# Kernel optimization log

Hardware: AMD Instinct MI355X
Metric: run time of the kernel (lower is better)

The kernel has to match this reference:

```python
import math
import jax, jax.numpy as jnp
import numpy as np

LMAX = 2


def _cg_complex(j1, m1, j2, m2, j3, m3):
    # Standard (Racah) Clebsch-Gordan coefficient <j1 m1 j2 m2 | j3 m3> for integer l.
    if m1 + m2 != m3 or j3 < abs(j1 - j2) or j3 > j1 + j2:
        return 0.0
    f = math.factorial
    pre = math.sqrt((2 * j3 + 1) * f(j3 + j1 - j2) * f(j3 - j1 + j2) * f(j1 + j2 - j3) / f(j1 + j2 + j3 + 1))
    pre *= math.sqrt(f(j3 + m3) * f(j3 - m3) * f(j1 - m1) * f(j1 + m1) * f(j2 - m2) * f(j2 + m2))
    kmin = max(0, j2 - j3 - m1, j1 + m2 - j3)
    kmax = min(j1 + j2 - j3, j1 - m1, j2 + m2)
    s = 0.0
    for k in range(kmin, kmax + 1):
        s += (-1.0) ** k / (f(k) * f(j1 + j2 - j3 - k) * f(j1 - m1 - k) * f(j2 + m2 - k) * f(j3 - j2 + m1 + k) * f(j3 - j1 - m2 + k))
    return pre * s


def _u_matrix(l):
    # Unitary map from complex SH (Condon-Shortley) to real SH, rows = real mu, cols = complex m.
    U = np.zeros((2 * l + 1, 2 * l + 1), dtype=np.complex128)
    U[l, l] = 1.0
    isq2 = 1.0 / math.sqrt(2.0)
    for m in range(1, l + 1):
        U[l + m, l - m] = isq2
        U[l + m, l + m] = ((-1.0) ** m) * isq2
        U[l - m, l - m] = 1j * isq2
        U[l - m, l + m] = -1j * ((-1.0) ** m) * isq2
    return U


def _real_clebsch_gordan(lmax):
    # Dense real-SH CG tensor over combined s=(l,m) indices, shape [S,S,S], S=(lmax+1)^2.
    S = (lmax + 1) ** 2
    cg = np.zeros((S, S, S))
    for l1 in range(lmax + 1):
        for l2 in range(lmax + 1):
            for l3 in range(abs(l1 - l2), min(lmax, l1 + l2) + 1):
                blk = np.zeros((2 * l1 + 1, 2 * l2 + 1, 2 * l3 + 1))
                for i1, m1 in enumerate(range(-l1, l1 + 1)):
                    for i2, m2 in enumerate(range(-l2, l2 + 1)):
                        for i3, m3 in enumerate(range(-l3, l3 + 1)):
                            blk[i1, i2, i3] = _cg_complex(l1, m1, l2, m2, l3, m3)
                U1, U2, U3 = _u_matrix(l1), _u_matrix(l2), _u_matrix(l3)
                r = np.einsum('am,bn,co,mno->abc', U1, U2, U3.conj(), blk.astype(np.complex128))
                r = r.real if (l1 + l2 + l3) % 2 == 0 else r.imag  # parity-dependent real part
                cg[l1 * l1:(l1 + 1) ** 2, l2 * l2:(l2 + 1) ** 2, l3 * l3:(l3 + 1) ** 2] = r
    return cg


def _sparse_cg(lmax):
    cg = _real_clebsch_gordan(lmax)
    i1, i2, i3 = np.nonzero(np.abs(cg) > 1e-10)
    vals = cg[i1, i2, i3].astype(np.float32)
    widx = np.floor(np.sqrt(i3.astype(np.float64))).astype(np.int32)  # l of output combined index
    return vals, i1.astype(np.int32), i2.astype(np.int32), i3.astype(np.int32), widx


def _spherical_harmonics_l2(d):
    # Real SH up to l=2, 'component' normalization (|x|=1 assumed). Order: (l,m) = (0,0),(1,-1),(1,0),(1,1),(2,-2..2).
    x, y, z = d[..., 0], d[..., 1], d[..., 2]
    s3, s5, s15 = math.sqrt(3.0), math.sqrt(5.0), math.sqrt(15.0)
    return jnp.stack([
        jnp.ones_like(x),
        s3 * y, s3 * z, s3 * x,
        s15 * x * y, s15 * y * z, 0.5 * s5 * (3.0 * z * z - 1.0), s15 * x * z, 0.5 * s15 * (x * x - y * y),
    ], axis=-1)


def setup_inputs():
    N_ATOMS, N_EDGES, N_BASIS, N_RADIAL = 1200, 12000, 128, 20
    S = (LMAX + 1) ** 2
    key = jax.random.key(0)
    ks = jax.random.split(key, 8)
    vals, i1, i2, i3, widx = _sparse_cg(LMAX)
    return {
        'x': jax.random.normal(ks[0], (N_ATOMS, S, N_BASIS), jnp.float32),
        'radial_ij': jax.random.uniform(ks[1], (N_EDGES, N_RADIAL), jnp.float32),
        'dir_ij': jax.random.normal(ks[2], (N_EDGES, 3), jnp.float32),
        'cutoff_ij': jax.random.uniform(ks[3], (N_EDGES, 1), jnp.float32),
        'W_filter': jax.random.normal(ks[6], (N_RADIAL, N_BASIS * (LMAX + 1)), jnp.float32) / math.sqrt(N_RADIAL),
        'b_filter': jnp.zeros((N_BASIS * (LMAX + 1),), jnp.float32),
        'cg_vals': jnp.asarray(vals),
        'idx_i': jax.random.randint(ks[4], (N_EDGES,), 0, N_ATOMS),
        'idx_j': jax.random.randint(ks[5], (N_EDGES,), 0, N_ATOMS),
        'cg_idx_in1': jnp.asarray(i1),
        'cg_idx_in2': jnp.asarray(i2),
        'cg_idx_out': jnp.asarray(i3),
        'w_idx': jnp.asarray(widx),
    }


def reference(x, radial_ij, dir_ij, cutoff_ij, W_filter, b_filter, cg_vals,
              idx_i, idx_j, cg_idx_in1, cg_idx_in2, cg_idx_out, w_idx):
    n_atoms, S, F = x.shape
    E = dir_ij.shape[0]
    d = dir_ij / jnp.linalg.norm(dir_ij, axis=-1, keepdims=True)
    Y = _spherical_harmonics_l2(d)                        # [E, S]
    Wij = (radial_ij @ W_filter + b_filter) * cutoff_ij   # [E, (lmax+1)*F]
    Wij = Wij.reshape(E, LMAX + 1, F)                     # per-l radial filter
    xj = x[idx_j]                                         # [E, S, F] neighbor features
    # Sparse CG tensor-product contraction over combined (l,m) indices.
    v = (Y[:, cg_idx_in2, None] * cg_vals[None, :, None]
         * Wij[:, w_idx, :] * xj[:, cg_idx_in1, :])       # [E, n_cg, F]
    yij = jnp.zeros((E, S, F), v.dtype).at[:, cg_idx_out, :].add(v)
    return jax.ops.segment_sum(yij, idx_i, num_segments=n_atoms)
```

## Files before the change

### kernel.cpp

```cpp
#include <hip/hip_runtime.h>
#include <math.h>


#define S9     9
#define MROW   12
#define MSZ    (S9 * MROW)
#define NF     128
#define NRAD   20
#define CEDGE  8
#define NCHUNK 3
#define CAP    64
#define NCELL  81
#define MAXCG  512

__device__ inline float2 f2fma(float a, float2 b, float2 c) {
    return make_float2(fmaf(a, b.x, c.x), fmaf(a, b.y, c.y));
}

__global__ __launch_bounds__(256) void prep_kernel(
    const int* __restrict__ idx_i, int E, int nbuck,
    const int* __restrict__ cg_i1, const int* __restrict__ cg_i2,
    const int* __restrict__ cg_i3, const float* __restrict__ cg_vals, int ncg,
    int* __restrict__ cnt,
    int* __restrict__ buck,
    int* __restrict__ cellOff,
    int2* __restrict__ cellDat)
{
    const int t = threadIdx.x;
    if ((int)blockIdx.x < nbuck) {
        int e = blockIdx.x * 256 + t;
        if (e < E) {
            int a = idx_i[e];
            int p = atomicAdd(&cnt[a], 1);
            if (p < CAP) buck[a * CAP + p] = e;
        }
        return;
    }
    __shared__ int hist[NCELL];
    __shared__ int cur[NCELL];
    if (t < NCELL) hist[t] = 0;
    __syncthreads();
    for (int k = t; k < ncg; k += 256)
        atomicAdd(&hist[cg_i3[k] * S9 + cg_i1[k]], 1);
    __syncthreads();
    if (t == 0) {
        int run = 0;
        for (int c = 0; c < NCELL; ++c) {
            cellOff[c] = run; cur[c] = run; run += hist[c];
        }
        cellOff[NCELL] = run;
    }
    __syncthreads();
    for (int k = t; k < ncg; k += 256) {
        int cell = cg_i3[k] * S9 + cg_i1[k];
        int p = atomicAdd(&cur[cell], 1);
        cellDat[p] = make_int2(cg_i2[k], __float_as_int(cg_vals[k]));
    }
}

__global__ __launch_bounds__(64) void so3_chunk_kernel(
    const float* __restrict__ x,
    const float* __restrict__ radial,
    const float* __restrict__ dir,
    const float* __restrict__ cutoff,
    const float* __restrict__ Wf,
    const float* __restrict__ bf,
    const int* __restrict__ idx_j,
    const int* __restrict__ cnt,
    const int* __restrict__ buck,
    const int* __restrict__ cellOff,
    const int2* __restrict__ cellDat,
    int ncg,
    float* __restrict__ slots)
{
    const int a = blockIdx.x / NCHUNK;
    const int q = blockIdx.x - a * NCHUNK;
    const int t = threadIdx.x;

    const int deg = min(cnt[a], CAP);
    if (q > 0 && q * CEDGE >= deg) return;

    __shared__ __align__(16) float M[CEDGE][MSZ];
    __shared__ float Ysh[CEDGE][S9];
    __shared__ float radsh[CEDGE][NRAD];
    __shared__ float cutsh[CEDGE];
    __shared__ int   egsh[CEDGE];
    __shared__ int   jsh[CEDGE];
    __shared__ int   offsh[NCELL + 1];
    __shared__ int2  datsh[MAXCG];

    for (int k = t; k <= NCELL; k += 64) offsh[k] = cellOff[k];
    for (int k = t; k < ncg; k += 64) datsh[k] = cellDat[k];

    float2 acc[S9];
    #pragma unroll
    for (int s = 0; s < S9; ++s) acc[s] = make_float2(0.f, 0.f);

    const float2 b0 = ((const float2*)(bf + 0 * NF))[t];
    const float2 b1 = ((const float2*)(bf + 1 * NF))[t];
    const float2 b2 = ((const float2*)(bf + 2 * NF))[t];

    int base = q * CEDGE;
    do {
        const int n = min(CEDGE, deg - base);

        if (t < CEDGE) {
            int e = 0, jj = a;
            float cut = 0.f;
            float y0 = 0.f, y1 = 0.f, y2 = 0.f, y3 = 0.f, y4 = 0.f,
                  y5 = 0.f, y6 = 0.f, y7 = 0.f, y8 = 0.f;
            if (t < n) {
                e = buck[a * CAP + base + t];
                jj = idx_j[e];
                cut = cutoff[e];
                float dx = dir[3 * e], dy = dir[3 * e + 1], dz = dir[3 * e + 2];
                const float inv = rsqrtf(dx * dx + dy * dy + dz * dz);
                dx *= inv; dy *= inv; dz *= inv;
                const float s3c  = 1.7320508075688772f;
                const float s5c  = 2.2360679774997896f;
                const float s15c = 3.8729833462074170f;
                y0 = 1.0f;
                y1 = s3c * dy; y2 = s3c * dz; y3 = s3c * dx;
                y4 = s15c * dx * dy; y5 = s15c * dy * dz;
                y6 = 0.5f * s5c * (3.0f * dz * dz - 1.0f);
                y7 = s15c * dx * dz;
                y8 = 0.5f * s15c * (dx * dx - dy * dy);
            }
            egsh[t] = e; jsh[t] = jj; cutsh[t] = cut;
            Ysh[t][0] = y0; Ysh[t][1] = y1; Ysh[t][2] = y2;
            Ysh[t][3] = y3; Ysh[t][4] = y4; Ysh[t][5] = y5;
            Ysh[t][6] = y6; Ysh[t][7] = y7; Ysh[t][8] = y8;
        }
        for (int qq = t; qq < CEDGE * NRAD; qq += 64) {
            const int c = qq / NRAD;
            const int r = qq - c * NRAD;
            float v = 0.f;
            if (c < n) v = radial[(size_t)egsh[c] * NRAD + r];
            radsh[c][r] = v;
        }

        float2 w[CEDGE][3];
        #pragma unroll
        for (int c = 0; c < CEDGE; ++c) { w[c][0] = b0; w[c][1] = b1; w[c][2] = b2; }
        #pragma unroll 4
        for (int r = 0; r < NRAD; ++r) {
            const float2* wrow = (const float2*)(Wf + r * (3 * NF));
            const float2 w0 = wrow[t];
            const float2 w1 = wrow[t + 64];
            const float2 w2 = wrow[t + 128];
            #pragma unroll
            for (int c = 0; c < CEDGE; ++c) {
                const float rv = radsh[c][r];
                w[c][0] = f2fma(rv, w0, w[c][0]);
                w[c][1] = f2fma(rv, w1, w[c][1]);
                w[c][2] = f2fma(rv, w2, w[c][2]);
            }
        }
        #pragma unroll
        for (int c = 0; c < CEDGE; ++c) {
            const float cut = cutsh[c];
            w[c][0].x *= cut; w[c][0].y *= cut;
            w[c][1].x *= cut; w[c][1].y *= cut;
            w[c][2].x *= cut; w[c][2].y *= cut;
        }

        #pragma unroll
        for (int cc = 0; cc < 2; ++cc) {
            const int cell = t + cc * 64;
            if (cell < NCELL) {
                const int s3i = cell / 9;
                const int s1i = cell - 9 * s3i;
                const int o0 = offsh[cell], o1 = offsh[cell + 1];
                float m[CEDGE];
                #pragma unroll
                for (int c = 0; c < CEDGE; ++c) m[c] = 0.f;
                for (int idx = o0; idx < o1; ++idx) {
                    const int2 d = datsh[idx];
                    const float v = __int_as_float(d.y);
                    #pragma unroll
                    for (int c = 0; c < CEDGE; ++c)
                        m[c] = fmaf(v, Ysh[c][d.x], m[c]);
                }
                #pragma unroll
                for (int c = 0; c < CEDGE; ++c) M[c][s3i * MROW + s1i] = m[c];
            }
        }

        #pragma unroll
        for (int c = 0; c < CEDGE; ++c) {
            const int j = __builtin_amdgcn_readfirstlane(jsh[c]);
            const float2* xp = (const float2*)(x + (size_t)j * (S9 * NF)) + t;
            float2 xj[S9];
            #pragma unroll
            for (int s = 0; s < S9; ++s) xj[s] = xp[s * 64];

            #pragma unroll
            for (int s3 = 0; s3 < S9; ++s3) {
                const float4* mr = (const float4*)&M[c][s3 * MROW];
                const float4 m0 = mr[0];
                const float4 m1 = mr[1];
                const float  m8 = M[c][s3 * MROW + 8];
                float2 tsum = make_float2(0.f, 0.f);
                tsum = f2fma(m0.x, xj[0], tsum);
                tsum = f2fma(m0.y, xj[1], tsum);
                tsum = f2fma(m0.z, xj[2], tsum);
                tsum = f2fma(m0.w, xj[3], tsum);
                tsum = f2fma(m1.x, xj[4], tsum);
                tsum = f2fma(m1.y, xj[5], tsum);
                tsum = f2fma(m1.z, xj[6], tsum);
                tsum = f2fma(m1.w, xj[7], tsum);
                tsum = f2fma(m8,   xj[8], tsum);
                const float2 wl = (s3 == 0) ? w[c][0] : ((s3 < 4) ? w[c][1] : w[c][2]);
                acc[s3].x = fmaf(wl.x, tsum.x, acc[s3].x);
                acc[s3].y = fmaf(wl.y, tsum.y, acc[s3].y);
            }
        }
        base += CEDGE;
    } while (q == NCHUNK - 1 && base < deg);

    float2* sp = (float2*)(slots + (size_t)(a * NCHUNK + q) * (S9 * NF)) + t;
    #pragma unroll
    for (int s = 0; s < S9; ++s) sp[s * 64] = acc[s];
}

__global__ __launch_bounds__(64) void reduce_kernel(
    const float* __restrict__ slots, const int* __restrict__ cnt,
    float* __restrict__ out)
{
    const int a = blockIdx.x;
    const int t = threadIdx.x;
    const int deg = min(cnt[a], CAP);
    const int nch = min((deg + CEDGE - 1) / CEDGE, NCHUNK);

    float2 acc[S9];
    #pragma unroll
    for (int s = 0; s < S9; ++s) acc[s] = make_float2(0.f, 0.f);

    for (int q = 0; q < nch; ++q) {
        const float2* sp = (const float2*)(slots + (size_t)(a * NCHUNK + q) * (S9 * NF)) + t;
        #pragma unroll
        for (int s = 0; s < S9; ++s) {
            float2 v = sp[s * 64];
            acc[s].x += v.x; acc[s].y += v.y;
        }
    }
    float2* op = (float2*)(out + (size_t)a * (S9 * NF)) + t;
    #pragma unroll
    for (int s = 0; s < S9; ++s) op[s * 64] = acc[s];
}

__global__ __launch_bounds__(256) void so3_edge_fused(
    const float* __restrict__ x, const float* __restrict__ radial,
    const float* __restrict__ dir, const float* __restrict__ cutoff,
    const float* __restrict__ Wf, const float* __restrict__ bf,
    const float* __restrict__ cg_vals,
    const int* __restrict__ idx_i, const int* __restrict__ idx_j,
    const int* __restrict__ cg_i1, const int* __restrict__ cg_i2,
    const int* __restrict__ cg_i3, int ncg, int E,
    float* __restrict__ out)
{
    const int wid  = threadIdx.x >> 6;
    const int lane = threadIdx.x & 63;
    const int e = blockIdx.x * 4 + wid;
    if (e >= E) return;

    __shared__ __align__(16) float Msh[4][MSZ];
    __shared__ float Ysh[4][S9];

    if (lane < 27) ((float4*)&Msh[wid][0])[lane] = make_float4(0.f, 0.f, 0.f, 0.f);

    float dx = dir[3 * e], dy = dir[3 * e + 1], dz = dir[3 * e + 2];
    const float inv = rsqrtf(dx * dx + dy * dy + dz * dz);
    dx *= inv; dy *= inv; dz *= inv;
    if (lane == 0) {
        const float s3c = 1.7320508075688772f, s5c = 2.2360679774997896f,
                    s15c = 3.8729833462074170f;
        Ysh[wid][0] = 1.0f;
        Ysh[wid][1] = s3c * dy; Ysh[wid][2] = s3c * dz; Ysh[wid][3] = s3c * dx;
        Ysh[wid][4] = s15c * dx * dy; Ysh[wid][5] = s15c * dy * dz;
        Ysh[wid][6] = 0.5f * s5c * (3.0f * dz * dz - 1.0f);
        Ysh[wid][7] = s15c * dx * dz;
        Ysh[wid][8] = 0.5f * s15c * (dx * dx - dy * dy);
    }
    for (int k = lane; k < ncg; k += 64)
        atomicAdd(&Msh[wid][cg_i3[k] * MROW + cg_i1[k]], cg_vals[k] * Ysh[wid][cg_i2[k]]);

    float rad[NRAD];
    #pragma unroll
    for (int r = 0; r < NRAD; ++r) rad[r] = radial[(size_t)e * NRAD + r];
    const float cut = cutoff[e];

    float2 w0 = ((const float2*)(bf + 0 * NF))[lane];
    float2 w1 = ((const float2*)(bf + 1 * NF))[lane];
    float2 w2 = ((const float2*)(bf + 2 * NF))[lane];
    #pragma unroll 4
    for (int r = 0; r < NRAD; ++r) {
        const float2* wrow = (const float2*)(Wf + r * (3 * NF));
        w0 = f2fma(rad[r], wrow[lane], w0);
        w1 = f2fma(rad[r], wrow[lane + 64], w1);
        w2 = f2fma(rad[r], wrow[lane + 128], w2);
    }
    w0.x *= cut; w0.y *= cut; w1.x *= cut; w1.y *= cut; w2.x *= cut; w2.y *= cut;

    const int j = __builtin_amdgcn_readfirstlane(idx_j[e]);
    const float2* xp = (const float2*)(x + (size_t)j * (S9 * NF)) + lane;
    float2 xj[S9];
    #pragma unroll
    for (int s = 0; s < S9; ++s) xj[s] = xp[s * 64];

    const int a = __builtin_amdgcn_readfirstlane(idx_i[e]);
    float* op = out + (size_t)a * (S9 * NF) + 2 * lane;
    #pragma unroll
    for (int s3 = 0; s3 < S9; ++s3) {
        const float4* mr = (const float4*)&Msh[wid][s3 * MROW];
        const float4 m0 = mr[0];
        const float4 m1 = mr[1];
        const float  m8 = Msh[wid][s3 * MROW + 8];
        float2 tsum = make_float2(0.f, 0.f);
        tsum = f2fma(m0.x, xj[0], tsum);
        tsum = f2fma(m0.y, xj[1], tsum);
        tsum = f2fma(m0.z, xj[2], tsum);
        tsum = f2fma(m0.w, xj[3], tsum);
        tsum = f2fma(m1.x, xj[4], tsum);
        tsum = f2fma(m1.y, xj[5], tsum);
        tsum = f2fma(m1.z, xj[6], tsum);
        tsum = f2fma(m1.w, xj[7], tsum);
        tsum = f2fma(m8,   xj[8], tsum);
        const float2 wl = (s3 == 0) ? w0 : ((s3 < 4) ? w1 : w2);
        atomicAdd(&op[s3 * NF],     wl.x * tsum.x);
        atomicAdd(&op[s3 * NF + 1], wl.y * tsum.y);
    }
}

extern "C" void kernel_launch(void* const* d_in, const int* in_sizes, int n_in,
                              void* d_out, int out_size, void* d_ws, size_t ws_size,
                              hipStream_t stream) {
    const float* x       = (const float*)d_in[0];
    const float* radial  = (const float*)d_in[1];
    const float* dir     = (const float*)d_in[2];
    const float* cutoff  = (const float*)d_in[3];
    const float* Wf      = (const float*)d_in[4];
    const float* bf      = (const float*)d_in[5];
    const float* cg_vals = (const float*)d_in[6];
    const int*   idx_i   = (const int*)d_in[7];
    const int*   idx_j   = (const int*)d_in[8];
    const int*   cg_i1   = (const int*)d_in[9];
    const int*   cg_i2   = (const int*)d_in[10];
    const int*   cg_i3   = (const int*)d_in[11];

    const int E   = in_sizes[7];
    const int ncg = in_sizes[6];
    const int A   = in_sizes[0] / (S9 * NF);

    int* cnt      = (int*)d_ws;
    int* cellOff  = cnt + A;
    int* buck     = cellOff + (NCELL + 1);
    size_t ib     = (size_t)(A + NCELL + 1 + A * CAP) * sizeof(int);
    size_t doff   = (ib + 255) & ~(size_t)255;
    int2* cellDat = (int2*)((char*)d_ws + doff);
    size_t soff   = (doff + (size_t)ncg * sizeof(int2) + 255) & ~(size_t)255;
    float* slots  = (float*)((char*)d_ws + soff);
    size_t need   = soff + (size_t)A * NCHUNK * (S9 * NF) * sizeof(float);

    if (ws_size >= need && ncg <= MAXCG) {
        hipMemsetAsync(cnt, 0, (size_t)A * sizeof(int), stream);

        const int nbuck = (E + 255) / 256;
        prep_kernel<<<nbuck + 1, 256, 0, stream>>>(
            idx_i, E, nbuck, cg_i1, cg_i2, cg_i3, cg_vals, ncg,
            cnt, buck, cellOff, cellDat);

        so3_chunk_kernel<<<A * NCHUNK, 64, 0, stream>>>(
            x, radial, dir, cutoff, Wf, bf, idx_j,
            cnt, buck, cellOff, cellDat, ncg, slots);

        reduce_kernel<<<A, 64, 0, stream>>>(slots, cnt, (float*)d_out);
    } else {
        hipMemsetAsync(d_out, 0, (size_t)out_size * sizeof(float), stream);
        so3_edge_fused<<<(E + 3) / 4, 256, 0, stream>>>(
            x, radial, dir, cutoff, Wf, bf, cg_vals, idx_i, idx_j,
            cg_i1, cg_i2, cg_i3, ncg, E, (float*)d_out);
    }
}
```

Before: 123.4 us.

## Pack four atom-chunk wavefronts per block to share the CG table load

The chunk kernel now runs four independent 64-lane wavefronts per 256-thread block, each handling its own (atom, chunk) pair with per-wave shared-memory slices. The CG cell offsets and data are loaded into shared memory once per block instead of once per wave, and block count drops by four. The reduce kernel is packed the same way. In exchange, shared memory per block roughly quadruples for the per-wave buffers, which may limit occupancy. An added block barrier makes all waves wait for the table load even when their chunk is inactive.

```diff
diff --git a/kernel.cpp b/kernel.cpp
--- a/kernel.cpp
+++ b/kernel.cpp
@@ -58,7 +58,7 @@
     }
 }
 
-__global__ __launch_bounds__(64) void so3_chunk_kernel(
+__global__ __launch_bounds__(256) void so3_chunk_kernel(
     const float* __restrict__ x,
     const float* __restrict__ radial,
     const float* __restrict__ dir,
@@ -70,47 +70,56 @@
     const int* __restrict__ buck,
     const int* __restrict__ cellOff,
     const int2* __restrict__ cellDat,
-    int ncg,
+    int ncg, int A,
     float* __restrict__ slots)
 {
-    const int a = blockIdx.x / NCHUNK;
-    const int q = blockIdx.x - a * NCHUNK;
-    const int t = threadIdx.x;
-
-    const int deg = min(cnt[a], CAP);
-    if (q > 0 && q * CEDGE >= deg) return;
-
-    __shared__ __align__(16) float M[CEDGE][MSZ];
-    __shared__ float Ysh[CEDGE][S9];
-    __shared__ float radsh[CEDGE][NRAD];
-    __shared__ float cutsh[CEDGE];
-    __shared__ int   egsh[CEDGE];
-    __shared__ int   jsh[CEDGE];
+    const int t    = threadIdx.x;
+    const int lane = t & 63;
+    const int wid  = t >> 6;
+    const int ch   = blockIdx.x * 4 + wid;
+
+    __shared__ __align__(16) float M[4][CEDGE][MSZ];
+    __shared__ float Ysh[4][CEDGE][S9];
+    __shared__ float radsh[4][CEDGE][NRAD];
+    __shared__ float cutsh[4][CEDGE];
+    __shared__ int   egsh[4][CEDGE];
+    __shared__ int   jsh[4][CEDGE];
     __shared__ int   offsh[NCELL + 1];
     __shared__ int2  datsh[MAXCG];
 
-    for (int k = t; k <= NCELL; k += 64) offsh[k] = cellOff[k];
-    for (int k = t; k < ncg; k += 64) datsh[k] = cellDat[k];
+    int a = 0, q = 0, deg = 0;
+    bool active = (ch < A * NCHUNK);
+    if (active) {
+        a = ch / NCHUNK;
+        q = ch - a * NCHUNK;
+        deg = min(cnt[a], CAP);
+        if (q > 0 && q * CEDGE >= deg) active = false;
+    }
+
+    for (int k = t; k <= NCELL; k += 256) offsh[k] = cellOff[k];
+    for (int k = t; k < ncg; k += 256) datsh[k] = cellDat[k];
+    __syncthreads();
+    if (!active) return;
 
     float2 acc[S9];
     #pragma unroll
     for (int s = 0; s < S9; ++s) acc[s] = make_float2(0.f, 0.f);
 
-    const float2 b0 = ((const float2*)(bf + 0 * NF))[t];
-    const float2 b1 = ((const float2*)(bf + 1 * NF))[t];
-    const float2 b2 = ((const float2*)(bf + 2 * NF))[t];
+    const float2 b0 = ((const float2*)(bf + 0 * NF))[lane];
+    const float2 b1 = ((const float2*)(bf + 1 * NF))[lane];
+    const float2 b2 = ((const float2*)(bf + 2 * NF))[lane];
 
     int base = q * CEDGE;
     do {
         const int n = min(CEDGE, deg - base);
 
-        if (t < CEDGE) {
+        if (lane < CEDGE) {
             int e = 0, jj = a;
             float cut = 0.f;
             float y0 = 0.f, y1 = 0.f, y2 = 0.f, y3 = 0.f, y4 = 0.f,
                   y5 = 0.f, y6 = 0.f, y7 = 0.f, y8 = 0.f;
-            if (t < n) {
-                e = buck[a * CAP + base + t];
+            if (lane < n) {
+                e = buck[a * CAP + base + lane];
                 jj = idx_j[e];
                 cut = cutoff[e];
                 float dx = dir[3 * e], dy = dir[3 * e + 1], dz = dir[3 * e + 2];
@@ -126,17 +135,17 @@
                 y7 = s15c * dx * dz;
                 y8 = 0.5f * s15c * (dx * dx - dy * dy);
             }
-            egsh[t] = e; jsh[t] = jj; cutsh[t] = cut;
-            Ysh[t][0] = y0; Ysh[t][1] = y1; Ysh[t][2] = y2;
-            Ysh[t][3] = y3; Ysh[t][4] = y4; Ysh[t][5] = y5;
-            Ysh[t][6] = y6; Ysh[t][7] = y7; Ysh[t][8] = y8;
-        }
-        for (int qq = t; qq < CEDGE * NRAD; qq += 64) {
+            egsh[wid][lane] = e; jsh[wid][lane] = jj; cutsh[wid][lane] = cut;
+            Ysh[wid][lane][0] = y0; Ysh[wid][lane][1] = y1; Ysh[wid][lane][2] = y2;
+            Ysh[wid][lane][3] = y3; Ysh[wid][lane][4] = y4; Ysh[wid][lane][5] = y5;
+            Ysh[wid][lane][6] = y6; Ysh[wid][lane][7] = y7; Ysh[wid][lane][8] = y8;
+        }
+        for (int qq = lane; qq < CEDGE * NRAD; qq += 64) {
             const int c = qq / NRAD;
             const int r = qq - c * NRAD;
             float v = 0.f;
-            if (c < n) v = radial[(size_t)egsh[c] * NRAD + r];
-            radsh[c][r] = v;
+            if (c < n) v = radial[(size_t)egsh[wid][c] * NRAD + r];
+            radsh[wid][c][r] = v;
         }
 
         float2 w[CEDGE][3];
@@ -145,12 +154,12 @@
         #pragma unroll 4
         for (int r = 0; r < NRAD; ++r) {
             const float2* wrow = (const float2*)(Wf + r * (3 * NF));
-            const float2 w0 = wrow[t];
-            const float2 w1 = wrow[t + 64];
-            const float2 w2 = wrow[t + 128];
+            const float2 w0 = wrow[lane];
+            const float2 w1 = wrow[lane + 64];
+            const float2 w2 = wrow[lane + 128];
             #pragma unroll
             for (int c = 0; c < CEDGE; ++c) {
-                const float rv = radsh[c][r];
+                const float rv = radsh[wid][c][r];
                 w[c][0] = f2fma(rv, w0, w[c][0]);
                 w[c][1] = f2fma(rv, w1, w[c][1]);
                 w[c][2] = f2fma(rv, w2, w[c][2]);
@@ -158,7 +167,7 @@
         }
         #pragma unroll
         for (int c = 0; c < CEDGE; ++c) {
-            const float cut = cutsh[c];
+            const float cut = cutsh[wid][c];
             w[c][0].x *= cut; w[c][0].y *= cut;
             w[c][1].x *= cut; w[c][1].y *= cut;
             w[c][2].x *= cut; w[c][2].y *= cut;
@@ -166,7 +175,7 @@
 
         #pragma unroll
         for (int cc = 0; cc < 2; ++cc) {
-            const int cell = t + cc * 64;
+            const int cell = lane + cc * 64;
             if (cell < NCELL) {
                 const int s3i = cell / 9;
                 const int s1i = cell - 9 * s3i;
@@ -179,27 +188,27 @@
                     const float v = __int_as_float(d.y);
                     #pragma unroll
                     for (int c = 0; c < CEDGE; ++c)
-                        m[c] = fmaf(v, Ysh[c][d.x], m[c]);
+                        m[c] = fmaf(v, Ysh[wid][c][d.x], m[c]);
                 }
                 #pragma unroll
-                for (int c = 0; c < CEDGE; ++c) M[c][s3i * MROW + s1i] = m[c];
+                for (int c = 0; c < CEDGE; ++c) M[wid][c][s3i * MROW + s1i] = m[c];
             }
         }
 
         #pragma unroll
         for (int c = 0; c < CEDGE; ++c) {
-            const int j = __builtin_amdgcn_readfirstlane(jsh[c]);
-            const float2* xp = (const float2*)(x + (size_t)j * (S9 * NF)) + t;
+            const int j = __builtin_amdgcn_readfirstlane(jsh[wid][c]);
+            const float2* xp = (const float2*)(x + (size_t)j * (S9 * NF)) + lane;
             float2 xj[S9];
             #pragma unroll
             for (int s = 0; s < S9; ++s) xj[s] = xp[s * 64];
 
             #pragma unroll
             for (int s3 = 0; s3 < S9; ++s3) {
-                const float4* mr = (const float4*)&M[c][s3 * MROW];
+                const float4* mr = (const float4*)&M[wid][c][s3 * MROW];
                 const float4 m0 = mr[0];
                 const float4 m1 = mr[1];
-                const float  m8 = M[c][s3 * MROW + 8];
+                const float  m8 = M[wid][c][s3 * MROW + 8];
                 float2 tsum = make_float2(0.f, 0.f);
                 tsum = f2fma(m0.x, xj[0], tsum);
                 tsum = f2fma(m0.y, xj[1], tsum);
@@ -218,17 +227,18 @@
         base += CEDGE;
     } while (q == NCHUNK - 1 && base < deg);
 
-    float2* sp = (float2*)(slots + (size_t)(a * NCHUNK + q) * (S9 * NF)) + t;
+    float2* sp = (float2*)(slots + (size_t)(a * NCHUNK + q) * (S9 * NF)) + lane;
     #pragma unroll
     for (int s = 0; s < S9; ++s) sp[s * 64] = acc[s];
 }
 
-__global__ __launch_bounds__(64) void reduce_kernel(
-    const float* __restrict__ slots, const int* __restrict__ cnt,
+__global__ __launch_bounds__(256) void reduce_kernel(
+    const float* __restrict__ slots, const int* __restrict__ cnt, int A,
     float* __restrict__ out)
 {
-    const int a = blockIdx.x;
-    const int t = threadIdx.x;
+    const int a = blockIdx.x * 4 + (threadIdx.x >> 6);
+    if (a >= A) return;
+    const int t = threadIdx.x & 63;
     const int deg = min(cnt[a], CAP);
     const int nch = min((deg + CEDGE - 1) / CEDGE, NCHUNK);
 
@@ -370,11 +380,12 @@
             idx_i, E, nbuck, cg_i1, cg_i2, cg_i3, cg_vals, ncg,
             cnt, buck, cellOff, cellDat);
 
-        so3_chunk_kernel<<<A * NCHUNK, 64, 0, stream>>>(
+        const int nch_total = A * NCHUNK;
+        so3_chunk_kernel<<<(nch_total + 3) / 4, 256, 0, stream>>>(
             x, radial, dir, cutoff, Wf, bf, idx_j,
-            cnt, buck, cellOff, cellDat, ncg, slots);
-
-        reduce_kernel<<<A, 64, 0, stream>>>(slots, cnt, (float*)d_out);
+            cnt, buck, cellOff, cellDat, ncg, A, slots);
+
+        reduce_kernel<<<(A + 3) / 4, 256, 0, stream>>>(slots, cnt, A, (float*)d_out);
     } else {
         hipMemsetAsync(d_out, 0, (size_t)out_size * sizeof(float), stream);
         so3_edge_fused<<<(E + 3) / 4, 256, 0, stream>>>(
```

New measurement: 132.8 us. +7.6%, slower.
